# Kernel tuning notes

Measured on AMD Instinct MI355X. Metric: run time of the kernel, lower is better.

Reference implementation:

```python
import jax, jax.numpy as jnp
import numpy as np

NUM_NODES = 15000


def _gcn_conv(x, W, b, src, dst, norm, num_nodes):
    # PyG GCNConv: x' = D^-1/2 (A + I) D^-1/2 (x W) + b
    h = x @ W                                   # [N, out]
    msg = h[src] * norm[:, None]                # gather + scale per edge
    out = jax.ops.segment_sum(msg, dst, num_segments=num_nodes)
    return out + b


def setup_inputs() -> dict:
    key = jax.random.key(0)
    ks = jax.random.split(key, 12)
    T = 100000
    E = 200000
    inp = {
        "x": jax.random.normal(ks[0], (NUM_NODES, 768), jnp.float32),
        "r_emb": jax.random.normal(ks[1], (T, 768), jnp.float32),
        "W1": jax.random.normal(ks[2], (768, 10), jnp.float32) * 0.05,
        "b1": jax.random.normal(ks[3], (10,), jnp.float32) * 0.05,
        "W2": jax.random.normal(ks[4], (10, 128), jnp.float32) * 0.05,
        "b2": jax.random.normal(ks[5], (128,), jnp.float32) * 0.05,
        "W_ih": jax.random.normal(ks[6], (512, 1024), jnp.float32) * 0.03,
        "W_hh": jax.random.normal(ks[7], (512, 128), jnp.float32) * 0.03,
        "b_ih": jax.random.normal(ks[8], (512,), jnp.float32) * 0.03,
        "b_hh": jax.random.normal(ks[9], (512,), jnp.float32) * 0.03,
        "edge_index": jax.random.randint(ks[10], (2, E), 0, NUM_NODES).astype(jnp.int64),
        "triples": jax.random.randint(ks[11], (T, 3), 0, NUM_NODES).astype(jnp.int64),
    }
    return inp


def reference(x, r_emb, W1, b1, W2, b2, W_ih, W_hh, b_ih, b_hh, edge_index, triples):
    N = x.shape[0]
    H = 128  # lstm hidden size
    # --- add self loops, symmetric GCN normalization ---
    loop = jnp.arange(N, dtype=edge_index.dtype)
    src = jnp.concatenate([edge_index[0], loop])
    dst = jnp.concatenate([edge_index[1], loop])
    deg = jax.ops.segment_sum(jnp.ones_like(dst, jnp.float32), dst, num_segments=N)
    dinv = jnp.where(deg > 0, jax.lax.rsqrt(deg), 0.0)
    norm = dinv[src] * dinv[dst]                      # [E+N]
    # --- 2-layer GCN ---
    h = jax.nn.relu(_gcn_conv(x, W1, b1, src, dst, norm, N))   # [N, 10]
    z = _gcn_conv(h, W2, b2, src, dst, norm, N)                # [N, 128]
    # --- per-triple LSTM scoring, batched (seq_len=1, zero init state) ---
    hvec = z[triples[:, 0]]                           # [T, 128]
    tvec = z[triples[:, 2]]                           # [T, 128]
    feat = jnp.concatenate([hvec, r_emb, tvec], axis=-1)       # [T, 1024]
    gates = feat @ W_ih.T + (b_ih + b_hh)             # [T, 512]; h0=0 so W_hh term vanishes
    i_g, f_g, g_g, o_g = jnp.split(gates, 4, axis=-1)  # torch gate order i,f,g,o
    c = jax.nn.sigmoid(i_g) * jnp.tanh(g_g)           # c0 = 0 -> forget term drops
    out = jax.nn.sigmoid(o_g) * jnp.tanh(c)           # [T, 128]
    score = jax.nn.sigmoid(jnp.sum(out, axis=-1))     # [T]
    return score
```

## Files before the change

kernel.cpp:

```cpp
#include <hip/hip_runtime.h>

#define NF 768
#define D1 10
#define D2 128
#define BM 64

typedef __attribute__((ext_vector_type(8))) short bf16x8;
typedef __attribute__((ext_vector_type(16))) float f32x16;

static __device__ __forceinline__ float sigf(float v){ return 1.0f/(1.0f+__expf(-v)); }
static __device__ __forceinline__ float tanhfast(float v){ return 2.0f/(1.0f+__expf(-2.0f*v)) - 1.0f; }
static __device__ __forceinline__ short f2bf(float f){
    unsigned u = __float_as_uint(f);
    u += 0x7fffu + ((u>>16)&1u);
    return (short)(u>>16);
}

static __device__ __forceinline__ short4 cvt4(float4 a){
    unsigned u0,u1;
    asm("v_cvt_pk_bf16_f32 %0, %1, %2" : "=v"(u0) : "v"(a.x), "v"(a.y));
    asm("v_cvt_pk_bf16_f32 %0, %1, %2" : "=v"(u1) : "v"(a.z), "v"(a.w));
    union { unsigned u[2]; short4 s; } r;
    r.u[0]=u0; r.u[1]=u1;
    return r.s;
}

__global__ void k_deg(const int* __restrict__ dst, int* __restrict__ cnt, int E){
    int e = blockIdx.x*256 + threadIdx.x;
    if(e<E) atomicAdd(&cnt[dst[e]], 1);
}

__global__ __launch_bounds__(256) void k_scan(const int* __restrict__ cnt,
                                              int* __restrict__ rowptr, int* __restrict__ rowcur,
                                              float* __restrict__ dinv, int N, int E){
    __shared__ int part[256];
    int t = threadIdx.x;
    int C = (N+255)/256;
    int lo = t*C, hi = lo+C; if(hi>N) hi=N; if(lo>N) lo=N;
    int s=0;
    for(int i=lo;i<hi;i++) s += cnt[i];
    part[t]=s;
    __syncthreads();
    if(t==0){
        int run=0;
        for(int i=0;i<256;i++){ int v=part[i]; part[i]=run; run+=v; }
        rowptr[N]=E;
    }
    __syncthreads();
    int run = part[t];
    for(int i=lo;i<hi;i++){
        rowptr[i]=run; rowcur[i]=run; run += cnt[i];
        dinv[i] = rsqrtf((float)cnt[i] + 1.0f);
    }
}

__global__ void k_fill(const int* __restrict__ src, const int* __restrict__ dst,
                       const float* __restrict__ dinv, int* __restrict__ rowcur,
                       int* __restrict__ esrc, float* __restrict__ enorm, int E){
    int e = blockIdx.x*256 + threadIdx.x;
    if(e>=E) return;
    int s=src[e], d=dst[e];
    int pos = atomicAdd(&rowcur[d], 1);
    esrc[pos]=s;
    enorm[pos]=dinv[s]*dinv[d];
}

__global__ __launch_bounds__(256) void k_h1(const float* __restrict__ x,
                                            const float* __restrict__ W1,
                                            float* __restrict__ h1, int N){
    __shared__ float wt[D1*NF];
    for(int idx=threadIdx.x; idx<NF*D1; idx+=256){
        int k=idx/D1, c=idx-k*D1;
        wt[c*NF+k]=W1[idx];
    }
    __syncthreads();
    int row = blockIdx.x*4 + (threadIdx.x>>6);
    int lane = threadIdx.x&63;
    if(row>=N) return;
    const float4* xr = (const float4*)(x + (size_t)row*NF);
    float acc[D1];
#pragma unroll
    for(int c=0;c<D1;c++) acc[c]=0.f;
#pragma unroll
    for(int i=0;i<3;i++){
        float4 v = xr[lane + 64*i];
#pragma unroll
        for(int c=0;c<D1;c++){
            float4 w = *(const float4*)&wt[c*NF + (lane+64*i)*4];
            acc[c] += v.x*w.x + v.y*w.y + v.z*w.z + v.w*w.w;
        }
    }
#pragma unroll
    for(int c=0;c<D1;c++){
        float v=acc[c];
#pragma unroll
        for(int off=32;off;off>>=1) v += __shfl_down(v,off,64);
        acc[c]=v;
    }
    if(lane==0){
#pragma unroll
        for(int c=0;c<D1;c++) h1[(size_t)row*D1+c]=acc[c];
    }
}

__global__ __launch_bounds__(128) void k_gh(const float* __restrict__ h1,
        const int* __restrict__ rowptr, const int* __restrict__ esrc,
        const float* __restrict__ enorm, const float* __restrict__ dinv,
        const float* __restrict__ b1, const float* __restrict__ W2,
        float* __restrict__ hz, int N){
    __shared__ float w2s[D1*D2];
    int tid = threadIdx.x;
    for(int i=tid;i<D1*D2;i+=128) w2s[i]=W2[i];
    __syncthreads();
    int node = blockIdx.x*2 + (tid>>6);
    int lane = tid&63;
    if(node>=N) return;
    int e0=rowptr[node], e1=rowptr[node+1];
    float acc[D1];
#pragma unroll
    for(int c=0;c<D1;c++) acc[c]=0.f;
    for(int e=e0+lane; e<e1; e+=64){
        int s=esrc[e]; float w=enorm[e];
        const float* hr = h1 + (size_t)s*D1;
#pragma unroll
        for(int c=0;c<D1;c++) acc[c] += hr[c]*w;
    }
#pragma unroll
    for(int c=0;c<D1;c++){
        float v=acc[c];
#pragma unroll
        for(int off=32;off;off>>=1) v += __shfl_down(v,off,64);
        acc[c] = __shfl(v, 0, 64);
    }
    float di=dinv[node], d2=di*di;
    const float* hr = h1 + (size_t)node*D1;
    float h[D1];
#pragma unroll
    for(int c=0;c<D1;c++){
        float v = acc[c] + hr[c]*d2 + b1[c];
        h[c] = v>0.f ? v : 0.f;
    }
    float o0=0.f, o1=0.f;
#pragma unroll
    for(int k=0;k<D1;k++){
        o0 += h[k]*w2s[k*D2 + lane];
        o1 += h[k]*w2s[k*D2 + 64 + lane];
    }
    hz[(size_t)node*D2 + lane]      = o0;
    hz[(size_t)node*D2 + 64 + lane] = o1;
}

__global__ __launch_bounds__(128) void k_gath2(const float* __restrict__ hz,
        const int* __restrict__ rowptr, const int* __restrict__ esrc,
        const float* __restrict__ enorm, const float* __restrict__ dinv,
        const float* __restrict__ b2, float* __restrict__ zbf, int N){
    int n = blockIdx.x;
    int c = threadIdx.x;
    int e0 = rowptr[n], e1 = rowptr[n+1];
    float di = dinv[n];
    float acc = hz[(size_t)n*D2+c]*di*di + b2[c];
    int e = e0;
    for(; e+1<e1; e+=2){
        int s0=esrc[e], s1=esrc[e+1];
        float w0=enorm[e], w1=enorm[e+1];
        acc += hz[(size_t)s0*D2+c]*w0 + hz[(size_t)s1*D2+c]*w1;
    }
    if(e<e1) acc += hz[(size_t)esrc[e]*D2+c]*enorm[e];
    zbf[(size_t)n*D2+c] = acc;
}

__global__ void k_wimgB(const float* __restrict__ Wih, ushort* __restrict__ img,
                        int* __restrict__ cnt, int N){
    int gid = blockIdx.x*256 + threadIdx.x;
    if(gid < N) cnt[gid] = 0;
    if(gid >= 12*64*64) return;
    int l = gid & 63;
    int ks16 = (gid>>6) & 63;
    int f = gid >> 12;
    int dd = l & 31, kb = l>>5;
    int wn = f/3, gi = f - wn*3;
    int gbase = (gi==0)?0:((gi==1)?256:384);
    int wrow = gbase + wn*32 + dd;
    int k = ks16*16 + kb*8;
    const float* p = Wih + (size_t)wrow*1024 + k;
    float4 v0=*(const float4*)p, v1=*(const float4*)(p+4);
    ushort o[8];
    o[0]=f2bf(v0.x); o[1]=f2bf(v0.y); o[2]=f2bf(v0.z); o[3]=f2bf(v0.w);
    o[4]=f2bf(v1.x); o[5]=f2bf(v1.y); o[6]=f2bf(v1.z); o[7]=f2bf(v1.w);
    *(int4*)(img + (size_t)gid*8) = *(int4*)o;
}

__global__ __launch_bounds__(256,2) void k_big(
    const float* __restrict__ remb, const ushort* __restrict__ img,
    const float* __restrict__ zbf, const float* __restrict__ b_ih,
    const float* __restrict__ b_hh, const int* __restrict__ trip,
    float* __restrict__ rowacc, int T)
{
    __shared__ ushort Ab[3][2*64*8];
    int tid=threadIdx.x, lane=tid&63, w=tid>>6;
    int l31=lane&31, lh=lane>>5;
    int t0=blockIdx.x*BM;

    const int arow = w*16 + (lane>>2);
    const int asub = lane&3;
    int tc = t0 + arow; if(tc>=T) tc=T-1;
    const float* pzh = zbf + (size_t)trip[3*tc]*D2   + asub*4;
    const float* prm = remb + (size_t)tc*NF          + asub*4;
    const float* pzt = zbf + (size_t)trip[3*tc+2]*D2 + asub*4;
    const int awoff = ((asub>>1)*64 + arow)*8 + (asub&1)*4;
    const int ar0 = (lh*64 + l31)*8;
    const int ar1 = (lh*64 + 32 + l31)*8;

    const ushort* wb0 = img + ((size_t)((w*3+0)*64)*64 + lane)*8;
    const ushort* wb1 = img + ((size_t)((w*3+1)*64)*64 + lane)*8;
    const ushort* wb2 = img + ((size_t)((w*3+2)*64)*64 + lane)*8;

    f32x16 acc[2][3];
    const f32x16 zer = {0,0,0,0,0,0,0,0,0,0,0,0,0,0,0,0};
#pragma unroll
    for(int m=0;m<2;m++)
#pragma unroll
        for(int g=0;g<3;g++) acc[m][g]=zer;

    float4 pa[4];
    bf16x8 qb[2][3];

#define ALOAD(C_) if((C_)<64){ \
    const float* s_; \
    if((C_)<8)       s_ = pzh + (C_)*16; \
    else if((C_)<56) s_ = prm + ((C_)-8)*16; \
    else             s_ = pzt + ((C_)-56)*16; \
    pa[(C_)&3] = *(const float4*)s_; }

#define AWRITE(C_) if((C_)<64){ \
    *(short4*)&Ab[(C_)%3][awoff] = cvt4(pa[(C_)&3]); }

#define BLOAD(C_) if((C_)<64){ \
    qb[(C_)&1][0] = *(const bf16x8*)(wb0 + (size_t)(C_)*512); \
    qb[(C_)&1][1] = *(const bf16x8*)(wb1 + (size_t)(C_)*512); \
    qb[(C_)&1][2] = *(const bf16x8*)(wb2 + (size_t)(C_)*512); }

#define CH(C_) { \
    BLOAD((C_)+1) \
    ALOAD((C_)+4) \
    __builtin_amdgcn_sched_barrier(0); \
    AWRITE((C_)+1) \
    asm volatile("s_waitcnt lgkmcnt(0)" ::: "memory"); \
    __builtin_amdgcn_s_barrier(); \
    __builtin_amdgcn_sched_barrier(0); \
    { \
        const ushort* a_ = &Ab[(C_)%3][0]; \
        bf16x8 A0_ = *(const bf16x8*)&a_[ar0]; \
        bf16x8 A1_ = *(const bf16x8*)&a_[ar1]; \
        bf16x8 B0_ = qb[(C_)&1][0]; \
        bf16x8 B1_ = qb[(C_)&1][1]; \
        bf16x8 B2_ = qb[(C_)&1][2]; \
        __builtin_amdgcn_s_setprio(1); \
        acc[0][0]=__builtin_amdgcn_mfma_f32_32x32x16_bf16(A0_,B0_,acc[0][0],0,0,0); \
        acc[0][1]=__builtin_amdgcn_mfma_f32_32x32x16_bf16(A0_,B1_,acc[0][1],0,0,0); \
        acc[0][2]=__builtin_amdgcn_mfma_f32_32x32x16_bf16(A0_,B2_,acc[0][2],0,0,0); \
        acc[1][0]=__builtin_amdgcn_mfma_f32_32x32x16_bf16(A1_,B0_,acc[1][0],0,0,0); \
        acc[1][1]=__builtin_amdgcn_mfma_f32_32x32x16_bf16(A1_,B1_,acc[1][1],0,0,0); \
        acc[1][2]=__builtin_amdgcn_mfma_f32_32x32x16_bf16(A1_,B2_,acc[1][2],0,0,0); \
        __builtin_amdgcn_s_setprio(0); \
    } \
}

    ALOAD(0) ALOAD(1) ALOAD(2) ALOAD(3)
    __builtin_amdgcn_sched_barrier(0);
    BLOAD(0)
    __builtin_amdgcn_sched_barrier(0);
    AWRITE(0)

    CH(0)  CH(1)  CH(2)  CH(3)  CH(4)  CH(5)  CH(6)  CH(7)
    CH(8)  CH(9)  CH(10) CH(11) CH(12) CH(13) CH(14) CH(15)
    CH(16) CH(17) CH(18) CH(19) CH(20) CH(21) CH(22) CH(23)
    CH(24) CH(25) CH(26) CH(27) CH(28) CH(29) CH(30) CH(31)
    CH(32) CH(33) CH(34) CH(35) CH(36) CH(37) CH(38) CH(39)
    CH(40) CH(41) CH(42) CH(43) CH(44) CH(45) CH(46) CH(47)
    CH(48) CH(49) CH(50) CH(51) CH(52) CH(53) CH(54) CH(55)
    CH(56) CH(57) CH(58) CH(59) CH(60) CH(61) CH(62) CH(63)
#undef CH
#undef BLOAD
#undef AWRITE
#undef ALOAD

    int d = w*32+l31;
    float bi=b_ih[d]+b_hh[d];
    float bg=b_ih[256+d]+b_hh[256+d];
    float bo=b_ih[384+d]+b_hh[384+d];
#pragma unroll
    for(int m=0;m<2;m++){
#pragma unroll
        for(int r=0;r<16;r++){
            int row = m*32 + (r&3)+8*(r>>2)+4*lh;
            int t = t0+row;
            float ov = 0.f;
            if(t<T){
                float ig = acc[m][0][r] + bi;
                float gg = acc[m][1][r] + bg;
                float og = acc[m][2][r] + bo;
                float cc = sigf(ig)*tanhfast(gg);
                ov = sigf(og)*tanhfast(cc);
            }
#pragma unroll
            for(int off=1; off<32; off<<=1) ov += __shfl_xor(ov, off, 64);
            if(l31==0 && t<T) atomicAdd(&rowacc[t], ov);
        }
    }
}

__global__ void k_sig(const float* __restrict__ rowacc, float* __restrict__ score, int T){
    int t = blockIdx.x*256 + threadIdx.x;
    if(t<T) score[t] = sigf(rowacc[t]);
}

extern "C" void kernel_launch(void* const* d_in, const int* in_sizes, int n_in,
                              void* d_out, int out_size, void* d_ws, size_t ws_size,
                              hipStream_t stream){
    const float* x    = (const float*)d_in[0];
    const float* remb = (const float*)d_in[1];
    const float* W1   = (const float*)d_in[2];
    const float* b1   = (const float*)d_in[3];
    const float* W2   = (const float*)d_in[4];
    const float* b2   = (const float*)d_in[5];
    const float* Wih  = (const float*)d_in[6];
    const float* b_ih = (const float*)d_in[8];
    const float* b_hh = (const float*)d_in[9];
    const int*   ei   = (const int*)d_in[10];
    const int*   trip = (const int*)d_in[11];
    float* score = (float*)d_out;

    const int N = in_sizes[0]/NF;
    const int E = in_sizes[10]/2;
    const int T = in_sizes[11]/3;
    const int* src = ei;
    const int* dst = ei + E;

    float* ws = (float*)d_ws;
    size_t o = 0;
    ushort* img   = (ushort*)(ws+o); o += (size_t)12*64*64*8/2;
    float* zbf    = ws+o;            o += (size_t)N*D2;
    float* rowacc = ws+o;            o += (size_t)((T+7)&~7);
    int*   cnt    = (int*)(ws+o);    o += (size_t)((N+8)&~7);
    int*   rowptr = (int*)(ws+o);    o += (size_t)((N+8)&~7);
    int*   rowcur = (int*)(ws+o);    o += (size_t)((N+8)&~7);
    int*   esrc   = (int*)(ws+o);    o += (size_t)E;
    float* enorm  = ws+o;            o += (size_t)E;
    float* dinv   = ws+o;            o += (size_t)((N+7)&~7);
    float* h1     = ws+o;            o += (size_t)N*D1;
    float* hz     = ws+o;            o += (size_t)N*D2;
    (void)ws_size; (void)n_in; (void)out_size;

    hipMemsetAsync(rowacc, 0, (size_t)T*sizeof(float), stream);

    k_wimgB<<<dim3((12*64*64+255)/256), dim3(256), 0, stream>>>(Wih, img, cnt, N);
    k_deg  <<<dim3((E+255)/256), dim3(256), 0, stream>>>(dst, cnt, E);
    k_scan <<<dim3(1), dim3(256), 0, stream>>>(cnt, rowptr, rowcur, dinv, N, E);
    k_fill <<<dim3((E+255)/256), dim3(256), 0, stream>>>(src, dst, dinv, rowcur, esrc, enorm, E);
    k_h1   <<<dim3((N+3)/4), dim3(256), 0, stream>>>(x, W1, h1, N);
    k_gh   <<<dim3((N+1)/2), dim3(128), 0, stream>>>(h1, rowptr, esrc, enorm, dinv, b1, W2, hz, N);
    k_gath2<<<dim3(N), dim3(128), 0, stream>>>(hz, rowptr, esrc, enorm, dinv, b2, zbf, N);
    k_big  <<<dim3((T+BM-1)/BM), dim3(256), 0, stream>>>(remb, img, zbf, b_ih, b_hh, trip, rowacc, T);
    k_sig  <<<dim3((T+255)/256), dim3(256), 0, stream>>>(rowacc, score, T);
}
```

Baseline: 306.6 us.

## Halve LSTM GEMM row tile to 32 and raise occupancy to 3 blocks

Shrinks the per-block triple tile in the fused gather+LSTM GEMM from 64 to 32 rows. Each wave now holds 3 accumulators instead of 6, and A-tile staging uses float2 loads. Launch bounds go from 2 to 3 blocks per CU to gain occupancy and more blocks. The cost is that the bf16 weight B-fragments are loaded from global memory twice as often relative to the MFMA work, with more barriers per useful FLOP.

```diff
diff --git a/kernel.cpp b/kernel.cpp
--- a/kernel.cpp
+++ b/kernel.cpp
@@ -3,7 +3,7 @@
 #define NF 768
 #define D1 10
 #define D2 128
-#define BM 64
+#define BM 32
 
 typedef __attribute__((ext_vector_type(8))) short bf16x8;
 typedef __attribute__((ext_vector_type(16))) float f32x16;
@@ -16,13 +16,10 @@
     return (short)(u>>16);
 }
 
-static __device__ __forceinline__ short4 cvt4(float4 a){
-    unsigned u0,u1;
-    asm("v_cvt_pk_bf16_f32 %0, %1, %2" : "=v"(u0) : "v"(a.x), "v"(a.y));
-    asm("v_cvt_pk_bf16_f32 %0, %1, %2" : "=v"(u1) : "v"(a.z), "v"(a.w));
-    union { unsigned u[2]; short4 s; } r;
-    r.u[0]=u0; r.u[1]=u1;
-    return r.s;
+static __device__ __forceinline__ short2 cvt2(float2 a){
+    unsigned u;
+    asm("v_cvt_pk_bf16_f32 %0, %1, %2" : "=v"(u) : "v"(a.x), "v"(a.y));
+    union { unsigned uu; short2 s; } r; r.uu=u; return r.s;
 }
 
 __global__ void k_deg(const int* __restrict__ dst, int* __restrict__ cnt, int E){
@@ -190,39 +187,34 @@
     *(int4*)(img + (size_t)gid*8) = *(int4*)o;
 }
 
-__global__ __launch_bounds__(256,2) void k_big(
+__global__ __launch_bounds__(256,3) void k_big(
     const float* __restrict__ remb, const ushort* __restrict__ img,
     const float* __restrict__ zbf, const float* __restrict__ b_ih,
     const float* __restrict__ b_hh, const int* __restrict__ trip,
     float* __restrict__ rowacc, int T)
 {
-    __shared__ ushort Ab[3][2*64*8];
+    __shared__ ushort Ab[3][2*32*8];
     int tid=threadIdx.x, lane=tid&63, w=tid>>6;
     int l31=lane&31, lh=lane>>5;
     int t0=blockIdx.x*BM;
 
-    const int arow = w*16 + (lane>>2);
-    const int asub = lane&3;
+    const int arow = tid>>3;
+    const int aseg = tid&7;
     int tc = t0 + arow; if(tc>=T) tc=T-1;
-    const float* pzh = zbf + (size_t)trip[3*tc]*D2   + asub*4;
-    const float* prm = remb + (size_t)tc*NF          + asub*4;
-    const float* pzt = zbf + (size_t)trip[3*tc+2]*D2 + asub*4;
-    const int awoff = ((asub>>1)*64 + arow)*8 + (asub&1)*4;
-    const int ar0 = (lh*64 + l31)*8;
-    const int ar1 = (lh*64 + 32 + l31)*8;
+    const float* pzh = zbf + (size_t)trip[3*tc]*D2   + aseg*2;
+    const float* prm = remb + (size_t)tc*NF          + aseg*2;
+    const float* pzt = zbf + (size_t)trip[3*tc+2]*D2 + aseg*2;
+    const int awoff = ((aseg>>2)*32 + arow)*8 + (aseg&3)*2;
+    const int ar = (lh*32 + l31)*8;
 
     const ushort* wb0 = img + ((size_t)((w*3+0)*64)*64 + lane)*8;
     const ushort* wb1 = img + ((size_t)((w*3+1)*64)*64 + lane)*8;
     const ushort* wb2 = img + ((size_t)((w*3+2)*64)*64 + lane)*8;
 
-    f32x16 acc[2][3];
     const f32x16 zer = {0,0,0,0,0,0,0,0,0,0,0,0,0,0,0,0};
-#pragma unroll
-    for(int m=0;m<2;m++)
-#pragma unroll
-        for(int g=0;g<3;g++) acc[m][g]=zer;
-
-    float4 pa[4];
+    f32x16 acc0=zer, acc1=zer, acc2=zer;
+
+    float2 pa[4];
     bf16x8 qb[2][3];
 
 #define ALOAD(C_) if((C_)<64){ \
@@ -230,10 +222,10 @@
     if((C_)<8)       s_ = pzh + (C_)*16; \
     else if((C_)<56) s_ = prm + ((C_)-8)*16; \
     else             s_ = pzt + ((C_)-56)*16; \
-    pa[(C_)&3] = *(const float4*)s_; }
+    pa[(C_)&3] = *(const float2*)s_; }
 
 #define AWRITE(C_) if((C_)<64){ \
-    *(short4*)&Ab[(C_)%3][awoff] = cvt4(pa[(C_)&3]); }
+    *(short2*)&Ab[(C_)%3][awoff] = cvt2(pa[(C_)&3]); }
 
 #define BLOAD(C_) if((C_)<64){ \
     qb[(C_)&1][0] = *(const bf16x8*)(wb0 + (size_t)(C_)*512); \
@@ -249,19 +241,14 @@
     __builtin_amdgcn_s_barrier(); \
     __builtin_amdgcn_sched_barrier(0); \
     { \
-        const ushort* a_ = &Ab[(C_)%3][0]; \
-        bf16x8 A0_ = *(const bf16x8*)&a_[ar0]; \
-        bf16x8 A1_ = *(const bf16x8*)&a_[ar1]; \
+        bf16x8 A_ = *(const bf16x8*)&Ab[(C_)%3][ar]; \
         bf16x8 B0_ = qb[(C_)&1][0]; \
         bf16x8 B1_ = qb[(C_)&1][1]; \
         bf16x8 B2_ = qb[(C_)&1][2]; \
         __builtin_amdgcn_s_setprio(1); \
-        acc[0][0]=__builtin_amdgcn_mfma_f32_32x32x16_bf16(A0_,B0_,acc[0][0],0,0,0); \
-        acc[0][1]=__builtin_amdgcn_mfma_f32_32x32x16_bf16(A0_,B1_,acc[0][1],0,0,0); \
-        acc[0][2]=__builtin_amdgcn_mfma_f32_32x32x16_bf16(A0_,B2_,acc[0][2],0,0,0); \
-        acc[1][0]=__builtin_amdgcn_mfma_f32_32x32x16_bf16(A1_,B0_,acc[1][0],0,0,0); \
-        acc[1][1]=__builtin_amdgcn_mfma_f32_32x32x16_bf16(A1_,B1_,acc[1][1],0,0,0); \
-        acc[1][2]=__builtin_amdgcn_mfma_f32_32x32x16_bf16(A1_,B2_,acc[1][2],0,0,0); \
+        acc0=__builtin_amdgcn_mfma_f32_32x32x16_bf16(A_,B0_,acc0,0,0,0); \
+        acc1=__builtin_amdgcn_mfma_f32_32x32x16_bf16(A_,B1_,acc1,0,0,0); \
+        acc2=__builtin_amdgcn_mfma_f32_32x32x16_bf16(A_,B2_,acc2,0,0,0); \
         __builtin_amdgcn_s_setprio(0); \
     } \
 }
@@ -290,23 +277,20 @@
     float bg=b_ih[256+d]+b_hh[256+d];
     float bo=b_ih[384+d]+b_hh[384+d];
 #pragma unroll
-    for(int m=0;m<2;m++){
-#pragma unroll
-        for(int r=0;r<16;r++){
-            int row = m*32 + (r&3)+8*(r>>2)+4*lh;
-            int t = t0+row;
-            float ov = 0.f;
-            if(t<T){
-                float ig = acc[m][0][r] + bi;
-                float gg = acc[m][1][r] + bg;
-                float og = acc[m][2][r] + bo;
-                float cc = sigf(ig)*tanhfast(gg);
-                ov = sigf(og)*tanhfast(cc);
-            }
-#pragma unroll
-            for(int off=1; off<32; off<<=1) ov += __shfl_xor(ov, off, 64);
-            if(l31==0 && t<T) atomicAdd(&rowacc[t], ov);
+    for(int r=0;r<16;r++){
+        int row = (r&3)+8*(r>>2)+4*lh;
+        int t = t0+row;
+        float ov = 0.f;
+        if(t<T){
+            float ig = acc0[r] + bi;
+            float gg = acc1[r] + bg;
+            float og = acc2[r] + bo;
+            float cc = sigf(ig)*tanhfast(gg);
+            ov = sigf(og)*tanhfast(cc);
         }
+#pragma unroll
+        for(int off=1; off<32; off<<=1) ov += __shfl_xor(ov, off, 64);
+        if(l31==0 && t<T) atomicAdd(&rowacc[t], ov);
     }
 }
 
```

Measured after the change: 347.1 us. +13.2%, slower.
